# Kernel tuning notes

Hardware: AMD Instinct MI355X
Metric: run time of the kernel (lower is better)

The kernel has to match this reference:

```python
import jax, jax.numpy as jnp
import numpy as np

B, I, H = 8192, 256, 1024


def setup_inputs() -> dict:
    key = jax.random.key(0)
    ks = jax.random.split(key, 12)
    s = 1.0 / np.sqrt(H)
    return {
        "x_t": jax.random.normal(ks[0], (B, I), jnp.float32),
        "h": jax.random.normal(ks[1], (B, H), jnp.float32),
        "c": jax.random.normal(ks[2], (B, H), jnp.float32),
        "t0": jnp.zeros((), jnp.float32),
        "t1": jnp.ones((), jnp.float32),
        # nn.LSTMCell params (PyTorch layout: [4H, in], gate order i,f,g,o)
        "W_ih": jax.random.uniform(ks[3], (4 * H, I), jnp.float32, -s, s),
        "W_hh": jax.random.uniform(ks[4], (4 * H, H), jnp.float32, -s, s),
        "b_ih": jax.random.uniform(ks[5], (4 * H,), jnp.float32, -s, s),
        "b_hh": jax.random.uniform(ks[6], (4 * H,), jnp.float32, -s, s),
        # f_node = Linear(H+1, H) -> tanh -> Linear(H, H)
        "W1": jax.random.uniform(ks[7], (H, H + 1), jnp.float32, -s, s),
        "b1": jax.random.uniform(ks[8], (H,), jnp.float32, -s, s),
        "W2": jax.random.uniform(ks[9], (H, H), jnp.float32, -s, s),
        "b2": jax.random.uniform(ks[10], (H,), jnp.float32, -s, s),
    }


def _lstm_cell(x, h, c, W_ih, W_hh, b_ih, b_hh):
    # gates: [B, 4H], PyTorch gate order i, f, g, o
    gates = x @ W_ih.T + b_ih + h @ W_hh.T + b_hh
    i, f, g, o = jnp.split(gates, 4, axis=1)
    c_next = jax.nn.sigmoid(f) * c + jax.nn.sigmoid(i) * jnp.tanh(g)
    h_next = jax.nn.sigmoid(o) * jnp.tanh(c_next)
    return h_next, c_next


def _f_node(t, h, W1, b1, W2, b2):
    # concat time column: [B, H+1]
    t_col = jnp.broadcast_to(t.astype(h.dtype).reshape(1, 1), (h.shape[0], 1))
    z = jnp.tanh(jnp.concatenate([h, t_col], axis=1) @ W1.T + b1)
    return z @ W2.T + b2


def reference(x_t, h, c, t0, t1, W_ih, W_hh, b_ih, b_hh, W1, b1, W2, b2):
    h_tilde, c_next = _lstm_cell(x_t, h, c, W_ih, W_hh, b_ih, b_hh)
    # fixed-step RK4: torchdyn odeint with t_span=[t0, t1] -> single step
    dt = t1 - t0
    f = lambda t, y: _f_node(t, y, W1, b1, W2, b2)
    k1 = f(t0, h_tilde)
    k2 = f(t0 + 0.5 * dt, h_tilde + 0.5 * dt * k1)
    k3 = f(t0 + 0.5 * dt, h_tilde + 0.5 * dt * k2)
    k4 = f(t0 + dt, h_tilde + dt * k3)
    h_next = h_tilde + (dt / 6.0) * (k1 + 2.0 * k2 + 2.0 * k3 + k4)
    return h_next, c_next
```

## Files before the change

kernel.cpp:

```cpp
#include <hip/hip_runtime.h>

typedef short           s16x8 __attribute__((ext_vector_type(8)));
typedef unsigned short  u16;
typedef unsigned short  u16x8 __attribute__((ext_vector_type(8)));
typedef float           f32x4 __attribute__((ext_vector_type(4)));

#define DB   8192
#define DI   256
#define DH   1024
#define D4H  4096
#define KXH  1280
#define NTG  (KXH / 64)

__device__ __forceinline__ u16 f2bf(float f) {
    unsigned u = __float_as_uint(f);
    u = (u + 0x7FFFu + ((u >> 16) & 1u)) >> 16;
    return (u16)u;
}
__device__ __forceinline__ float bf2f(u16 v) {
    return __uint_as_float(((unsigned)v) << 16);
}
__device__ __forceinline__ float rcp_(float x) { return __builtin_amdgcn_rcpf(x); }
__device__ __forceinline__ float sigmoid_(float x) {
    x = fminf(fmaxf(x, -30.f), 30.f);
    return rcp_(1.0f + __expf(-x));
}
__device__ __forceinline__ float tanh_(float x) {
    x = fminf(fmaxf(x, -15.f), 15.f);
    float e = __expf(2.0f * x);
    return (e - 1.0f) * rcp_(e + 1.0f);
}
__device__ __forceinline__ void gload16(const void* g, void* l) {
    __builtin_amdgcn_global_load_lds(
        (const __attribute__((address_space(1))) unsigned int*)g,
        (__attribute__((address_space(3))) unsigned int*)l, 16, 0, 0);
}
__device__ __forceinline__ void barrier_() {
    asm volatile("" ::: "memory");
    __builtin_amdgcn_s_barrier();
    asm volatile("" ::: "memory");
}

__global__ __launch_bounds__(512, 2) void k_gates8(
    const u16* __restrict__ xh, const u16* __restrict__ Wg,
    const float* __restrict__ bsum, const float* __restrict__ cin,
    float* __restrict__ outc, u16* __restrict__ htl)
{
    __shared__ u16 lds[65536];

    const int t    = threadIdx.x;
    const int lane = t & 63;
    const int w    = t >> 6;
    const int wm   = w >> 2;
    const int wn   = w & 3;
    const int l15  = lane & 15;
    const int lg   = lane >> 4;
    const int swz  = l15 & 7;

    const int lin = blockIdx.y * 32 + blockIdx.x;
    const int sl  = (lin & 7) * 64 + (lin >> 3);
    const int m0  = (sl & 31) * 256;
    const int n0  = (sl >> 5) * 256;

    f32x4 acc[8][4];
    {   f32x4 z4 = {0.f, 0.f, 0.f, 0.f};
#pragma unroll
        for (int i = 0; i < 8; ++i)
#pragma unroll
            for (int j = 0; j < 4; ++j) acc[i][j] = z4;
    }

    const int r0 = t >> 3,        c80 = (t & 7) ^ (r0 & 7);
    const int r1 = (512 + t) >> 3, c81 = (t & 7) ^ (r1 & 7);
    const u16* gA0 = xh + (size_t)(m0 + r0) * KXH + c80 * 8;
    const u16* gA1 = xh + (size_t)(m0 + r1) * KXH + c81 * 8;
    const u16* gB0 = Wg + (size_t)(n0 + r0) * KXH + c80 * 8;
    const u16* gB1 = Wg + (size_t)(n0 + r1) * KXH + c81 * 8;
    u16* lw0 = lds + w * 512;

#define STAGE8(ab, h, tau) do {                                              \
        int tc_ = (tau) < NTG ? (tau) : NTG - 1;                             \
        int bo_ = ((tau) & 1) * 32768 + (ab) * 16384 + (h) * 8192;           \
        const u16* s0_ = ((ab) ? gB0 : gA0) + (size_t)(h) * 128 * KXH + tc_ * 64; \
        const u16* s1_ = ((ab) ? gB1 : gA1) + (size_t)(h) * 128 * KXH + tc_ * 64; \
        gload16(s0_, lw0 + bo_);                                             \
        gload16(s1_, lw0 + bo_ + 4096);                                      \
    } while (0)

    const int uK0  = (lg ^ swz) * 8;
    const int uK1  = ((4 + lg) ^ swz) * 8;
    const int aoff = (wm * 128 + l15) * 64;
    const int boff = (wn * 64 + l15) * 64;

#define RD_A8(a)                                                             \
    _Pragma("unroll") for (int mi = 0; mi < 4; ++mi) {                       \
        const u16* p_ = bufA + aoff + ((a) * 64 + mi * 16) * 64;             \
        av[mi][0] = *(const s16x8*)(p_ + uK0);                               \
        av[mi][1] = *(const s16x8*)(p_ + uK1);                               \
    }
#define RD_B8(b, bvv)                                                        \
    _Pragma("unroll") for (int ni = 0; ni < 2; ++ni) {                       \
        const u16* p_ = bufB + boff + ((b) * 32 + ni * 16) * 64;             \
        bvv[ni][0] = *(const s16x8*)(p_ + uK0);                              \
        bvv[ni][1] = *(const s16x8*)(p_ + uK1);                              \
    }
#define MFMA_Q8(ar, bc, bvv)                                                 \
    __builtin_amdgcn_s_setprio(1);                                           \
    _Pragma("unroll") for (int mi = 0; mi < 4; ++mi)                         \
    _Pragma("unroll") for (int ni = 0; ni < 2; ++ni) {                       \
        acc[(ar) + mi][(bc) + ni] = __builtin_amdgcn_mfma_f32_16x16x32_bf16( \
            av[mi][0], bvv[ni][0], acc[(ar) + mi][(bc) + ni], 0, 0, 0);      \
        acc[(ar) + mi][(bc) + ni] = __builtin_amdgcn_mfma_f32_16x16x32_bf16( \
            av[mi][1], bvv[ni][1], acc[(ar) + mi][(bc) + ni], 0, 0, 0);      \
    }                                                                        \
    __builtin_amdgcn_s_setprio(0);

    STAGE8(0, 0, 0); STAGE8(0, 1, 0); STAGE8(1, 0, 0); STAGE8(1, 1, 0);
    STAGE8(1, 0, 1); STAGE8(0, 0, 1);
    asm volatile("s_waitcnt vmcnt(4)" ::: "memory");
    __builtin_amdgcn_s_barrier();
    asm volatile("" ::: "memory");

    for (int tt = 0; tt < NTG; ++tt) {
        const u16* bufA = lds + (tt & 1) * 32768;
        const u16* bufB = bufA + 16384;
        s16x8 av[4][2], bv0[2][2], bv1[2][2];
        RD_A8(0); RD_B8(0, bv0);
        STAGE8(0, 1, tt + 1);
        barrier_();
        MFMA_Q8(0, 0, bv0);
        barrier_();
        RD_B8(1, bv1);
        STAGE8(1, 1, tt + 1);
        barrier_();
        MFMA_Q8(0, 2, bv1);
        barrier_();
        RD_A8(1);
        STAGE8(1, 0, tt + 2);
        barrier_();
        MFMA_Q8(4, 0, bv0);
        barrier_();
        STAGE8(0, 0, tt + 2);
        barrier_();
        MFMA_Q8(4, 2, bv1);
        asm volatile("s_waitcnt vmcnt(4)" ::: "memory");
        barrier_();
    }

    const int hb = ((n0 + wn * 64) >> 6) * 16 + l15;
    const int cb = n0 + wn * 64 + l15;
    const float bi = bsum[cb];
    const float bf = bsum[cb + 16];
    const float bg = bsum[cb + 32];
    const float bo = bsum[cb + 48];
#pragma unroll
    for (int mb = 0; mb < 8; ++mb) {
#pragma unroll
        for (int r = 0; r < 4; ++r) {
            const int m = m0 + wm * 128 + mb * 16 + lg * 4 + r;
            const size_t idx = (size_t)m * DH + hb;
            float iv = acc[mb][0][r] + bi;
            float fv = acc[mb][1][r] + bf;
            float gv = acc[mb][2][r] + bg;
            float ov = acc[mb][3][r] + bo;
            float cn = sigmoid_(fv) * cin[idx] + sigmoid_(iv) * tanh_(gv);
            outc[idx] = cn;
            htl[idx] = f2bf(sigmoid_(ov) * tanh_(cn));
        }
        __builtin_amdgcn_sched_barrier(0);
    }
#undef STAGE8
#undef RD_A8
#undef RD_B8
#undef MFMA_Q8
}

template<int KTOT, int BM, int BN>
__device__ __forceinline__ void gemm_tile(
    const u16* __restrict__ A, int lda,
    const u16* __restrict__ Bw, int ldb,
    int m0, int n0, u16* As, u16* Bs,
    f32x4 (&acc)[BM / 32][BN / 32])
{
    constexpr int MI = BM / 32, NI = BN / 32;
    const int t    = threadIdx.x;
    const int lane = t & 63;
    const int w    = t >> 6;
    const int wrr  = (w >> 1) * (BM / 2);
    const int wcc  = (w & 1) * (BN / 2);

    const int rr  = t >> 3;
    const int sc8 = (t & 7) ^ (rr & 7);
    const u16* gA = A  + (size_t)(m0 + rr) * lda + sc8 * 8;
    const u16* gB = Bw + (size_t)(n0 + rr) * ldb + sc8 * 8;
    u16* lA = As + w * 512;
    u16* lB = Bs + w * 512;

    const int l15 = lane & 15;
    const int lg  = lane >> 4;
    const int swz = l15 & 7;
    const char* cA = (const char*)As;
    const char* cB = (const char*)Bs;
    const int roA = (wrr + l15) * 128;
    const int roB = (wcc + l15) * 128;
    const int c0  = ((0 + lg) ^ swz) * 16;
    const int c1  = ((4 + lg) ^ swz) * 16;

    for (int kt = 0; kt < KTOT; kt += 64) {
#pragma unroll
        for (int q = 0; q < BM / 32; ++q)
            gload16(gA + (size_t)q * 32 * lda, lA + q * 2048);
#pragma unroll
        for (int q = 0; q < BN / 32; ++q)
            gload16(gB + (size_t)q * 32 * ldb, lB + q * 2048);
        gA += 64; gB += 64;
        __syncthreads();

#pragma unroll
        for (int ks = 0; ks < 2; ++ks) {
            const int cc = ks ? c1 : c0;
            s16x8 av[MI], bv[NI];
#pragma unroll
            for (int mi = 0; mi < MI; ++mi)
                av[mi] = *(const s16x8*)(cA + roA + mi * 2048 + cc);
#pragma unroll
            for (int ni = 0; ni < NI; ++ni)
                bv[ni] = *(const s16x8*)(cB + roB + ni * 2048 + cc);
#pragma unroll
            for (int mi = 0; mi < MI; ++mi)
#pragma unroll
                for (int ni = 0; ni < NI; ++ni)
                    acc[mi][ni] = __builtin_amdgcn_mfma_f32_16x16x32_bf16(
                        av[mi], bv[ni], acc[mi][ni], 0, 0, 0);
        }
        __syncthreads();
    }
}

#define GEMM_PROLOGUE(BM, BN)                                      \
    __shared__ u16 As[(BM) * 64], Bs[(BN) * 64];                   \
    f32x4 acc[(BM) / 32][(BN) / 32];                               \
    {   f32x4 z4 = {0.f, 0.f, 0.f, 0.f};                           \
        _Pragma("unroll") for (int i = 0; i < (BM) / 32; ++i)      \
        _Pragma("unroll") for (int j = 0; j < (BN) / 32; ++j)      \
            acc[i][j] = z4; }                                      \
    const int m0 = blockIdx.x * (BM), n0 = blockIdx.y * (BN);      \
    const int lane = threadIdx.x & 63, w = threadIdx.x >> 6;       \
    const int wrr = (w >> 1) * ((BM) / 2),                         \
              wcc = (w & 1) * ((BN) / 2);                          \
    const int l15 = lane & 15, lg = lane >> 4;

#define GEMM_PROLOGUE_SWZ(BM, BN)                                  \
    __shared__ u16 As[(BM) * 64], Bs[(BN) * 64];                   \
    f32x4 acc[(BM) / 32][(BN) / 32];                               \
    {   f32x4 z4 = {0.f, 0.f, 0.f, 0.f};                           \
        _Pragma("unroll") for (int i = 0; i < (BM) / 32; ++i)      \
        _Pragma("unroll") for (int j = 0; j < (BN) / 32; ++j)      \
            acc[i][j] = z4; }                                      \
    const int lin_ = blockIdx.y * 64 + blockIdx.x;                 \
    const int sl_  = (lin_ & 7) * 64 + (lin_ >> 3);                \
    const int m0 = (sl_ & 63) * (BM), n0 = (sl_ >> 6) * (BN);      \
    const int lane = threadIdx.x & 63, w = threadIdx.x >> 6;       \
    const int wrr = (w >> 1) * ((BM) / 2),                         \
              wcc = (w & 1) * ((BN) / 2);                          \
    const int l15 = lane & 15, lg = lane >> 4;

#define EPILOGUE_LOOP(MI, NI, BODY)                                \
    _Pragma("unroll") for (int mi = 0; mi < (MI); ++mi) {          \
    _Pragma("unroll") for (int ni = 0; ni < (NI); ++ni)            \
    _Pragma("unroll") for (int r = 0; r < 4; ++r) {                \
        const int m = m0 + wrr + mi * 16 + lg * 4 + r;             \
        const int n = n0 + wcc + ni * 16 + l15;                    \
        float v = acc[mi][ni][r];                                  \
        BODY                                                       \
    }                                                              \
    __builtin_amdgcn_sched_barrier(0); }

__global__ __launch_bounds__(256) void k_wc(
    const u16* __restrict__ W1z, const u16* __restrict__ W2t, u16* __restrict__ wc)
{
    GEMM_PROLOGUE(64, 128);
    gemm_tile<DH, 64, 128>(W1z, DH, W2t, DH, m0, n0, As, Bs, acc);
    EPILOGUE_LOOP(2, 4, { wc[(size_t)m * DH + n] = f2bf(v); })
}

__global__ __launch_bounds__(256) void k_gemm_u(
    const u16* __restrict__ htl, const u16* __restrict__ W1z,
    const float* __restrict__ cvA,
    u16* __restrict__ ubuf, u16* __restrict__ z1)
{
    GEMM_PROLOGUE_SWZ(128, 128);
    gemm_tile<DH, 128, 128>(htl, DH, W1z, DH, m0, n0, As, Bs, acc);
    EPILOGUE_LOOP(4, 4, {
        size_t idx = (size_t)m * DH + n;
        ubuf[idx] = f2bf(v);
        z1[idx] = f2bf(tanh_(v + cvA[n]));
    })
}

template<int IS4>
__global__ __launch_bounds__(256) void k_gemm_s(
    const u16* __restrict__ zin, const u16* __restrict__ wc,
    const u16* __restrict__ ubuf, const float* __restrict__ cv,
    const float* __restrict__ t0p, const float* __restrict__ t1p, float alpha,
    u16* __restrict__ zout,
    const u16* __restrict__ z1, const u16* __restrict__ z2,
    u16* __restrict__ Sb)
{
    GEMM_PROLOGUE_SWZ(128, 128);
    gemm_tile<DH, 128, 128>(zin, DH, wc, DH, m0, n0, As, Bs, acc);
    const float ad = alpha * (*t1p - *t0p);
    EPILOGUE_LOOP(4, 4, {
        size_t idx = (size_t)m * DH + n;
        float zz = tanh_(bf2f(ubuf[idx]) + ad * v + cv[n]);
        if (IS4) {
            Sb[idx] = f2bf(bf2f(z1[idx]) + 2.f * bf2f(z2[idx])
                           + 2.f * bf2f(zin[idx]) + zz);
        } else {
            zout[idx] = f2bf(zz);
        }
    })
}

__global__ __launch_bounds__(256) void k_gemm_h(
    const u16* __restrict__ Sb, const u16* __restrict__ W2b,
    const float* __restrict__ b2, const u16* __restrict__ htl,
    const float* __restrict__ t0p, const float* __restrict__ t1p,
    float* __restrict__ outh)
{
    GEMM_PROLOGUE_SWZ(128, 128);
    gemm_tile<DH, 128, 128>(Sb, DH, W2b, DH, m0, n0, As, Bs, acc);
    const float dtv = *t1p - *t0p;
    EPILOGUE_LOOP(4, 4, {
        size_t idx = (size_t)m * DH + n;
        outh[idx] = bf2f(htl[idx]) + (dtv * (1.0f / 6.0f)) * (v + 6.0f * b2[n]);
    })
}

#define NW   (D4H * (KXH / 8))
#define NBS  (D4H / 8)
#define NR1  (DH * (DH / 8))
#define NW2  (DH * (DH / 8))
#define NT2  (DH * (DH / 8))
#define NXH  (DB * (KXH / 8))
#define NCVW (DH * 64)
#define NPREP (NW + NBS + NR1 + NW2 + NT2 + NXH + NCVW)

__global__ __launch_bounds__(256) void k_prep_all(
    const float* __restrict__ x, const float* __restrict__ h,
    const float* __restrict__ Wih, const float* __restrict__ Whh,
    const float* __restrict__ bih, const float* __restrict__ bhh,
    const float* __restrict__ W1, const float* __restrict__ b1,
    const float* __restrict__ W2, const float* __restrict__ b2,
    const float* __restrict__ t0p, const float* __restrict__ t1p,
    u16* __restrict__ Wg, float* __restrict__ bsum,
    u16* __restrict__ W1z, u16* __restrict__ W2b, u16* __restrict__ W2t,
    float* __restrict__ cvA, float* __restrict__ cvB, float* __restrict__ cvC,
    u16* __restrict__ xh)
{
    int idx = blockIdx.x * 256 + threadIdx.x;
    if (idx < NW) {
        int n  = idx / (KXH / 8);
        int k8 = idx - n * (KXH / 8);
        int ro = ((n >> 4) & 3) * DH + (n >> 6) * 16 + (n & 15);
        const float* s = (k8 < DI / 8) ? (Wih + (size_t)ro * DI + k8 * 8)
                                       : (Whh + (size_t)ro * DH + (k8 - DI / 8) * 8);
        f32x4 x0 = *(const f32x4*)s;
        f32x4 x1 = *(const f32x4*)(s + 4);
        u16x8 o;
#pragma unroll
        for (int e = 0; e < 4; ++e) { o[e] = f2bf(x0[e]); o[e + 4] = f2bf(x1[e]); }
        *(u16x8*)(Wg + (size_t)idx * 8) = o;
        return;
    }
    idx -= NW;
    if (idx < NBS) {
#pragma unroll
        for (int e = 0; e < 8; ++e) {
            int n = idx * 8 + e;
            int ro = ((n >> 4) & 3) * DH + (n >> 6) * 16 + (n & 15);
            bsum[n] = bih[ro] + bhh[ro];
        }
        return;
    }
    idx -= NBS;
    if (idx < NR1) {
        int n = idx >> 7, k8 = idx & 127;
        const float* s = W1 + (size_t)n * (DH + 1) + k8 * 8;
        u16x8 o;
#pragma unroll
        for (int e = 0; e < 8; ++e) o[e] = f2bf(s[e]);
        *(u16x8*)(W1z + (size_t)idx * 8) = o;
        return;
    }
    idx -= NR1;
    if (idx < NW2) {
        const float* s = W2 + (size_t)idx * 8;
        f32x4 x0 = *(const f32x4*)s;
        f32x4 x1 = *(const f32x4*)(s + 4);
        u16x8 o;
#pragma unroll
        for (int e = 0; e < 4; ++e) { o[e] = f2bf(x0[e]); o[e + 4] = f2bf(x1[e]); }
        *(u16x8*)(W2b + (size_t)idx * 8) = o;
        return;
    }
    idx -= NW2;
    if (idx < NT2) {
        int i = idx >> 7, j8 = (idx & 127) * 8;
        u16x8 o;
#pragma unroll
        for (int e = 0; e < 8; ++e) o[e] = f2bf(W2[(size_t)(j8 + e) * DH + i]);
        *(u16x8*)(W2t + (size_t)i * DH + j8) = o;
        return;
    }
    idx -= NT2;
    if (idx < NXH) {
        int b  = idx / (KXH / 8);
        int k8 = idx - b * (KXH / 8);
        const float* s = (k8 < DI / 8) ? (x + (size_t)b * DI + k8 * 8)
                                       : (h + (size_t)b * DH + (k8 - DI / 8) * 8);
        f32x4 x0 = *(const f32x4*)s;
        f32x4 x1 = *(const f32x4*)(s + 4);
        u16x8 o;
#pragma unroll
        for (int e = 0; e < 4; ++e) { o[e] = f2bf(x0[e]); o[e + 4] = f2bf(x1[e]); }
        *(u16x8*)(xh + (size_t)idx * 8) = o;
        return;
    }
    idx -= NXH;
    if (idx < NCVW) {
        const int n    = idx >> 6;
        const int lane = idx & 63;
        const float* r = W1 + (size_t)n * (DH + 1);
        float s = 0.f;
#pragma unroll
        for (int j = 0; j < DH; j += 64)
            s += r[j + lane] * b2[j + lane];
#pragma unroll
        for (int d = 32; d >= 1; d >>= 1)
            s += __shfl_xor(s, d, 64);
        if (lane == 0) {
            const float t0v = *t0p, t1v = *t1p;
            const float dtv = t1v - t0v, tmv = t0v + 0.5f * dtv;
            const float wtn = r[DH];
            const float b1n = b1[n];
            cvA[n] = b1n + t0v * wtn;
            cvB[n] = 0.5f * dtv * s + b1n + tmv * wtn;
            cvC[n] = dtv * s + b1n + t1v * wtn;
        }
    }
}

extern "C" void kernel_launch(void* const* d_in, const int* in_sizes, int n_in,
                              void* d_out, int out_size, void* d_ws, size_t ws_size,
                              hipStream_t stream)
{
    (void)in_sizes; (void)n_in; (void)out_size;
    const float* x_t = (const float*)d_in[0];
    const float* hin = (const float*)d_in[1];
    const float* cin = (const float*)d_in[2];
    const float* t0p = (const float*)d_in[3];
    const float* t1p = (const float*)d_in[4];
    const float* Wih = (const float*)d_in[5];
    const float* Whh = (const float*)d_in[6];
    const float* bih = (const float*)d_in[7];
    const float* bhh = (const float*)d_in[8];
    const float* W1  = (const float*)d_in[9];
    const float* b1  = (const float*)d_in[10];
    const float* W2  = (const float*)d_in[11];
    const float* b2  = (const float*)d_in[12];

    char* ws = (char*)d_ws;
    size_t off = 0;
    u16*   Wg    = (u16*)(ws + off);  off += (size_t)D4H * KXH * 2;
    u16*   W1z   = (u16*)(ws + off);  off += (size_t)DH * DH * 2;
    u16*   W2b   = (u16*)(ws + off);  off += (size_t)DH * DH * 2;
    u16*   W2t   = (u16*)(ws + off);  off += (size_t)DH * DH * 2;
    u16*   wc    = (u16*)(ws + off);  off += (size_t)DH * DH * 2;
    float* bsum  = (float*)(ws + off); off += (size_t)D4H * 4;
    float* cvA   = (float*)(ws + off); off += (size_t)DH * 4;
    float* cvB   = (float*)(ws + off); off += (size_t)DH * 4;
    float* cvC   = (float*)(ws + off); off += (size_t)DH * 4;
    u16*   xh    = (u16*)(ws + off);  off += (size_t)DB * KXH * 2;
    u16*   htl   = (u16*)(ws + off);  off += (size_t)DB * DH * 2;
    u16*   ubuf  = (u16*)(ws + off);  off += (size_t)DB * DH * 2;
    u16*   z1    = (u16*)(ws + off);  off += (size_t)DB * DH * 2;
    u16*   z2    = (u16*)(ws + off);  off += (size_t)DB * DH * 2;
    u16*   z3    = (u16*)(ws + off);  off += (size_t)DB * DH * 2;
    u16*   Sb    = (u16*)(ws + off);  off += (size_t)DB * DH * 2;
    if (ws_size < off) return;

    float* outh = (float*)d_out;
    float* outc = outh + (size_t)DB * DH;

    k_prep_all<<<(NPREP + 255) / 256, 256, 0, stream>>>(
        x_t, hin, Wih, Whh, bih, bhh, W1, b1, W2, b2, t0p, t1p,
        Wg, bsum, W1z, W2b, W2t, cvA, cvB, cvC, xh);

    k_wc<<<dim3(DH / 64, DH / 128), 256, 0, stream>>>(W1z, W2t, wc);

    k_gates8<<<dim3(DB / 256, D4H / 256), 512, 0, stream>>>(
        xh, Wg, bsum, cin, outc, htl);

    dim3 gf(DB / 128, DH / 128);
    k_gemm_u<<<gf, 256, 0, stream>>>(htl, W1z, cvA, ubuf, z1);
    k_gemm_s<0><<<gf, 256, 0, stream>>>(z1, wc, ubuf, cvB, t0p, t1p, 0.5f,
                                        z2, nullptr, nullptr, nullptr);
    k_gemm_s<0><<<gf, 256, 0, stream>>>(z2, wc, ubuf, cvB, t0p, t1p, 0.5f,
                                        z3, nullptr, nullptr, nullptr);
    k_gemm_s<1><<<gf, 256, 0, stream>>>(z3, wc, ubuf, cvC, t0p, t1p, 1.0f,
                                        nullptr, z1, z2, Sb);
    k_gemm_h<<<gf, 256, 0, stream>>>(Sb, W2b, b2, htl, t0p, t1p, outh);
}
```

Before: 287.4 us.

## Fold weight-product GEMM into first RK stage kernel and drop block swizzles

Removes the separate k_wc launch by adding an extra row of 64 blocks to k_gemm_u that computes the W1z·W2t product with 128x128 tiles alongside the first-stage GEMM. It also removes the L2-oriented block-index swizzle from k_gates8 and the RK GEMM kernels, reverting to plain blockIdx mapping. The intent is to save a launch and its tail. The risk is lower L2 reuse from the linear tile order and some load imbalance from the extra blocks.

```diff
diff --git a/kernel.cpp b/kernel.cpp
--- a/kernel.cpp
+++ b/kernel.cpp
@@ -57,10 +57,8 @@
     const int lg   = lane >> 4;
     const int swz  = l15 & 7;
 
-    const int lin = blockIdx.y * 32 + blockIdx.x;
-    const int sl  = (lin & 7) * 64 + (lin >> 3);
-    const int m0  = (sl & 31) * 256;
-    const int n0  = (sl >> 5) * 256;
+    const int m0 = blockIdx.x * 256;
+    const int n0 = blockIdx.y * 256;
 
     f32x4 acc[8][4];
     {   f32x4 z4 = {0.f, 0.f, 0.f, 0.f};
@@ -250,21 +248,6 @@
               wcc = (w & 1) * ((BN) / 2);                          \
     const int l15 = lane & 15, lg = lane >> 4;
 
-#define GEMM_PROLOGUE_SWZ(BM, BN)                                  \
-    __shared__ u16 As[(BM) * 64], Bs[(BN) * 64];                   \
-    f32x4 acc[(BM) / 32][(BN) / 32];                               \
-    {   f32x4 z4 = {0.f, 0.f, 0.f, 0.f};                           \
-        _Pragma("unroll") for (int i = 0; i < (BM) / 32; ++i)      \
-        _Pragma("unroll") for (int j = 0; j < (BN) / 32; ++j)      \
-            acc[i][j] = z4; }                                      \
-    const int lin_ = blockIdx.y * 64 + blockIdx.x;                 \
-    const int sl_  = (lin_ & 7) * 64 + (lin_ >> 3);                \
-    const int m0 = (sl_ & 63) * (BM), n0 = (sl_ >> 6) * (BN);      \
-    const int lane = threadIdx.x & 63, w = threadIdx.x >> 6;       \
-    const int wrr = (w >> 1) * ((BM) / 2),                         \
-              wcc = (w & 1) * ((BN) / 2);                          \
-    const int l15 = lane & 15, lg = lane >> 4;
-
 #define EPILOGUE_LOOP(MI, NI, BODY)                                \
     _Pragma("unroll") for (int mi = 0; mi < (MI); ++mi) {          \
     _Pragma("unroll") for (int ni = 0; ni < (NI); ++ni)            \
@@ -276,26 +259,36 @@
     }                                                              \
     __builtin_amdgcn_sched_barrier(0); }
 
-__global__ __launch_bounds__(256) void k_wc(
-    const u16* __restrict__ W1z, const u16* __restrict__ W2t, u16* __restrict__ wc)
-{
-    GEMM_PROLOGUE(64, 128);
-    gemm_tile<DH, 64, 128>(W1z, DH, W2t, DH, m0, n0, As, Bs, acc);
-    EPILOGUE_LOOP(2, 4, { wc[(size_t)m * DH + n] = f2bf(v); })
-}
-
 __global__ __launch_bounds__(256) void k_gemm_u(
     const u16* __restrict__ htl, const u16* __restrict__ W1z,
-    const float* __restrict__ cvA,
-    u16* __restrict__ ubuf, u16* __restrict__ z1)
-{
-    GEMM_PROLOGUE_SWZ(128, 128);
-    gemm_tile<DH, 128, 128>(htl, DH, W1z, DH, m0, n0, As, Bs, acc);
-    EPILOGUE_LOOP(4, 4, {
-        size_t idx = (size_t)m * DH + n;
-        ubuf[idx] = f2bf(v);
-        z1[idx] = f2bf(tanh_(v + cvA[n]));
-    })
+    const u16* __restrict__ W2t, const float* __restrict__ cvA,
+    u16* __restrict__ ubuf, u16* __restrict__ z1, u16* __restrict__ wcout)
+{
+    __shared__ u16 As[128 * 64], Bs[128 * 64];
+    f32x4 acc[4][4];
+    {   f32x4 z4 = {0.f, 0.f, 0.f, 0.f};
+#pragma unroll
+        for (int i = 0; i < 4; ++i)
+#pragma unroll
+            for (int j = 0; j < 4; ++j) acc[i][j] = z4;
+    }
+    const int lane = threadIdx.x & 63, w = threadIdx.x >> 6;
+    const int wrr = (w >> 1) * 64, wcc = (w & 1) * 64;
+    const int l15 = lane & 15, lg = lane >> 4;
+
+    if (blockIdx.y < 8) {
+        const int m0 = blockIdx.x * 128, n0 = blockIdx.y * 128;
+        gemm_tile<DH, 128, 128>(htl, DH, W1z, DH, m0, n0, As, Bs, acc);
+        EPILOGUE_LOOP(4, 4, {
+            size_t idx = (size_t)m * DH + n;
+            ubuf[idx] = f2bf(v);
+            z1[idx] = f2bf(tanh_(v + cvA[n]));
+        })
+    } else {
+        const int m0 = (blockIdx.x & 7) * 128, n0 = (blockIdx.x >> 3) * 128;
+        gemm_tile<DH, 128, 128>(W1z, DH, W2t, DH, m0, n0, As, Bs, acc);
+        EPILOGUE_LOOP(4, 4, { wcout[(size_t)m * DH + n] = f2bf(v); })
+    }
 }
 
 template<int IS4>
@@ -307,7 +300,7 @@
     const u16* __restrict__ z1, const u16* __restrict__ z2,
     u16* __restrict__ Sb)
 {
-    GEMM_PROLOGUE_SWZ(128, 128);
+    GEMM_PROLOGUE(128, 128);
     gemm_tile<DH, 128, 128>(zin, DH, wc, DH, m0, n0, As, Bs, acc);
     const float ad = alpha * (*t1p - *t0p);
     EPILOGUE_LOOP(4, 4, {
@@ -328,7 +321,7 @@
     const float* __restrict__ t0p, const float* __restrict__ t1p,
     float* __restrict__ outh)
 {
-    GEMM_PROLOGUE_SWZ(128, 128);
+    GEMM_PROLOGUE(128, 128);
     gemm_tile<DH, 128, 128>(Sb, DH, W2b, DH, m0, n0, As, Bs, acc);
     const float dtv = *t1p - *t0p;
     EPILOGUE_LOOP(4, 4, {
@@ -497,13 +490,13 @@
         x_t, hin, Wih, Whh, bih, bhh, W1, b1, W2, b2, t0p, t1p,
         Wg, bsum, W1z, W2b, W2t, cvA, cvB, cvC, xh);
 
-    k_wc<<<dim3(DH / 64, DH / 128), 256, 0, stream>>>(W1z, W2t, wc);
-
     k_gates8<<<dim3(DB / 256, D4H / 256), 512, 0, stream>>>(
         xh, Wg, bsum, cin, outc, htl);
 
+    k_gemm_u<<<dim3(DB / 128, DH / 128 + 1), 256, 0, stream>>>(
+        htl, W1z, W2t, cvA, ubuf, z1, wc);
+
     dim3 gf(DB / 128, DH / 128);
-    k_gemm_u<<<gf, 256, 0, stream>>>(htl, W1z, cvA, ubuf, z1);
     k_gemm_s<0><<<gf, 256, 0, stream>>>(z1, wc, ubuf, cvB, t0p, t1p, 0.5f,
                                         z2, nullptr, nullptr, nullptr);
     k_gemm_s<0><<<gf, 256, 0, stream>>>(z2, wc, ubuf, cvB, t0p, t1p, 0.5f,
```

New measurement: 272.5 us. -5.2%, faster.
